# Kernel tuning notes

Measured on AMD Instinct MI355X. Metric: run time of the kernel, lower is better.

Reference implementation:

```python
import jax, jax.numpy as jnp
import numpy as np

B = 4194304  # batch size

def _ry(theta):
    # RY(theta) = [[cos(t/2), -sin(t/2)], [sin(t/2), cos(t/2)]], per-sample -> [B,2,2]
    c = jnp.cos(theta * 0.5)
    s = jnp.sin(theta * 0.5)
    return jnp.stack([jnp.stack([c, -s], -1), jnp.stack([s, c], -1)], -2)

def setup_inputs() -> dict:
    key = jax.random.key(0)
    k1, k2 = jax.random.split(key)
    x = jax.random.normal(k1, (B, 2), dtype=jnp.float32)
    parameters = jax.random.normal(k2, (B, 4), dtype=jnp.float32)
    return {"x": x, "parameters": parameters}

def reference(x, parameters):
    # RY(x0)RY(p0) on q0 == RY(x0+p0); same for q1. State is real throughout.
    a = x[:, 0] + parameters[:, 0]  # qubit 0 angle
    b = x[:, 1] + parameters[:, 1]  # qubit 1 angle
    ca, sa = jnp.cos(a * 0.5), jnp.sin(a * 0.5)
    cb, sb = jnp.cos(b * 0.5), jnp.sin(b * 0.5)
    # state[b, j1, j0] (qiskit little-endian: q0 is last axis)
    state = jnp.stack([
        jnp.stack([cb * ca, cb * sa], -1),
        jnp.stack([sb * ca, sb * sa], -1),
    ], -2)  # [B, 2, 2]
    # CX(control=q0, target=q1): flip j1 where j0 == 1
    state = jnp.stack([
        jnp.stack([state[:, 0, 0], state[:, 1, 1]], -1),
        jnp.stack([state[:, 1, 0], state[:, 0, 1]], -1),
    ], -2)
    # RY(p2) on q0 (last axis), RY(p3) on q1 (middle axis)
    R2 = _ry(parameters[:, 2])
    R3 = _ry(parameters[:, 3])
    state = jnp.einsum('bij,bkj->bki', R2, state)
    state = jnp.einsum('bij,bjk->bik', R3, state)
    probs = state * state  # real amplitudes -> probabilities
    z0 = probs[:, :, 0].sum(-1) - probs[:, :, 1].sum(-1)  # <Z> on qubit 0
    z1 = probs[:, 0, :].sum(-1) - probs[:, 1, :].sum(-1)  # <Z> on qubit 1
    return jnp.stack([z0, z1], -1)  # [B, 2]
```

## Files before the change

### kernel.cpp

```cpp
#include <hip/hip_runtime.h>


__device__ __forceinline__ float2 qsample(float x0, float x1, float4 p) {
    float sa, ca, sb, cb, s2, c2, s3, c3;
    __sincosf((x0 + p.x) * 0.5f, &sa, &ca);
    __sincosf((x1 + p.y) * 0.5f, &sb, &cb);
    __sincosf(p.z * 0.5f, &s2, &c2);
    __sincosf(p.w * 0.5f, &s3, &c3);

    float s00 = cb * ca;
    float s01 = sb * sa;
    float s10 = sb * ca;
    float s11 = cb * sa;

    float t00 = c2 * s00 - s2 * s01;
    float t01 = s2 * s00 + c2 * s01;
    float t10 = c2 * s10 - s2 * s11;
    float t11 = s2 * s10 + c2 * s11;

    float u00 = c3 * t00 - s3 * t10;
    float u01 = c3 * t01 - s3 * t11;
    float u10 = s3 * t00 + c3 * t10;
    float u11 = s3 * t01 + c3 * t11;

    float p00 = u00 * u00, p01 = u01 * u01, p10 = u10 * u10, p11 = u11 * u11;
    float z0 = (p00 + p10) - (p01 + p11);
    float z1 = (p00 + p01) - (p10 + p11);
    return make_float2(z0, z1);
}

__global__ void __launch_bounds__(256)
quantum_layer_kernel(const float4* __restrict__ x2,
                     const float4* __restrict__ p4,
                     float4* __restrict__ out2,
                     int npairs) {
    int i = blockIdx.x * blockDim.x + threadIdx.x;
    if (i >= npairs) return;

    float4 xv = x2[i];
    float4 pa = p4[2 * i + 0];
    float4 pb = p4[2 * i + 1];

    float2 za = qsample(xv.x, xv.y, pa);
    float2 zb = qsample(xv.z, xv.w, pb);

    out2[i] = make_float4(za.x, za.y, zb.x, zb.y);
}

extern "C" void kernel_launch(void* const* d_in, const int* in_sizes, int n_in,
                              void* d_out, int out_size, void* d_ws, size_t ws_size,
                              hipStream_t stream) {
    const float4* x2 = (const float4*)d_in[0];
    const float4* p4 = (const float4*)d_in[1];
    float4* out2 = (float4*)d_out;

    int B = in_sizes[0] / 2;
    int npairs = B / 2;
    int block = 256;
    int grid = (npairs + block - 1) / block;
    quantum_layer_kernel<<<grid, block, 0, stream>>>(x2, p4, out2, npairs);
}
```

Measured before the change: 127.2 us.

## Simplify expectation math to closed form, process four samples per thread, nontemporal stores

Replaces the explicit state-vector simulation with closed-form expressions for <Z0> and <Z1> that use full-angle sincos, so no half-angle multiplies or amplitude products are needed. Each thread now handles four samples instead of two, halving the thread count. Outputs are written with nontemporal stores to avoid polluting cache. The kernel is memory-bound on about 128 MB of traffic, so the reduced arithmetic and the store hint may matter little, and the wider per-thread work reduces parallelism.

```diff
diff --git a/kernel.cpp b/kernel.cpp
--- a/kernel.cpp
+++ b/kernel.cpp
@@ -1,50 +1,43 @@
 #include <hip/hip_runtime.h>
 
 
+typedef float vfloat4 __attribute__((ext_vector_type(4)));
+
 __device__ __forceinline__ float2 qsample(float x0, float x1, float4 p) {
-    float sa, ca, sb, cb, s2, c2, s3, c3;
-    __sincosf((x0 + p.x) * 0.5f, &sa, &ca);
-    __sincosf((x1 + p.y) * 0.5f, &sb, &cb);
-    __sincosf(p.z * 0.5f, &s2, &c2);
-    __sincosf(p.w * 0.5f, &s3, &c3);
-
-    float s00 = cb * ca;
-    float s01 = sb * sa;
-    float s10 = sb * ca;
-    float s11 = cb * sa;
-
-    float t00 = c2 * s00 - s2 * s01;
-    float t01 = s2 * s00 + c2 * s01;
-    float t10 = c2 * s10 - s2 * s11;
-    float t11 = s2 * s10 + c2 * s11;
-
-    float u00 = c3 * t00 - s3 * t10;
-    float u01 = c3 * t01 - s3 * t11;
-    float u10 = s3 * t00 + c3 * t10;
-    float u11 = s3 * t01 + c3 * t11;
-
-    float p00 = u00 * u00, p01 = u01 * u01, p10 = u10 * u10, p11 = u11 * u11;
-    float z0 = (p00 + p10) - (p01 + p11);
-    float z1 = (p00 + p01) - (p10 + p11);
+    float sa, ca, sb, cb, sc, cc, sd, cd;
+    __sincosf(x0 + p.x, &sa, &ca);
+    __sincosf(x1 + p.y, &sb, &cb);
+    __sincosf(p.z, &sc, &cc);
+    __sincosf(p.w, &sd, &cd);
+    float z0 = fmaf(ca, cc, -sa * sb * sc);
+    float z1 = fmaf(ca * cb, cd, -sb * sd);
     return make_float2(z0, z1);
 }
 
 __global__ void __launch_bounds__(256)
 quantum_layer_kernel(const float4* __restrict__ x2,
                      const float4* __restrict__ p4,
-                     float4* __restrict__ out2,
-                     int npairs) {
+                     vfloat4* __restrict__ out2,
+                     int nquads) {
     int i = blockIdx.x * blockDim.x + threadIdx.x;
-    if (i >= npairs) return;
+    if (i >= nquads) return;
 
-    float4 xv = x2[i];
-    float4 pa = p4[2 * i + 0];
-    float4 pb = p4[2 * i + 1];
+    float4 xa = x2[2 * i + 0];
+    float4 xb = x2[2 * i + 1];
+    float4 pa = p4[4 * i + 0];
+    float4 pb = p4[4 * i + 1];
+    float4 pc = p4[4 * i + 2];
+    float4 pd = p4[4 * i + 3];
 
-    float2 za = qsample(xv.x, xv.y, pa);
-    float2 zb = qsample(xv.z, xv.w, pb);
+    float2 z0 = qsample(xa.x, xa.y, pa);
+    float2 z1 = qsample(xa.z, xa.w, pb);
+    float2 z2 = qsample(xb.x, xb.y, pc);
+    float2 z3 = qsample(xb.z, xb.w, pd);
 
-    out2[i] = make_float4(za.x, za.y, zb.x, zb.y);
+    vfloat4 o0 = {z0.x, z0.y, z1.x, z1.y};
+    vfloat4 o1 = {z2.x, z2.y, z3.x, z3.y};
+    __builtin_nontemporal_store(o0, &out2[2 * i + 0]);
+    __builtin_nontemporal_store(o1, &out2[2 * i + 1]);
 }
 
 extern "C" void kernel_launch(void* const* d_in, const int* in_sizes, int n_in,
@@ -52,11 +45,11 @@
                               hipStream_t stream) {
     const float4* x2 = (const float4*)d_in[0];
     const float4* p4 = (const float4*)d_in[1];
-    float4* out2 = (float4*)d_out;
+    vfloat4* out2 = (vfloat4*)d_out;
 
     int B = in_sizes[0] / 2;
-    int npairs = B / 2;
+    int nquads = B / 4;
     int block = 256;
-    int grid = (npairs + block - 1) / block;
-    quantum_layer_kernel<<<grid, block, 0, stream>>>(x2, p4, out2, npairs);
+    int grid = (nquads + block - 1) / block;
+    quantum_layer_kernel<<<grid, block, 0, stream>>>(x2, p4, out2, nquads);
 }
```

Result: no change. 128.6 us (+1.1%).
